# Kernel optimization log

Hardware: AMD Instinct MI355X
Metric: run time of the kernel (lower is better)

## Reference

```python
import jax, jax.numpy as jnp
import numpy as np

LRELU_SLOPE = 0.2  # PyG GATConv default negative_slope
LN_EPS = 1e-5


def _layer_norm(x, g, b):
    mu = x.mean(-1, keepdims=True)
    var = x.var(-1, keepdims=True)
    return (x - mu) / jnp.sqrt(var + LN_EPS) * g + b


def _gat_conv(x, src, dst, W, a_src, a_dst, bias, heads, out_c, concat):
    # PyG GATConv (eval mode, self-loops already appended to src/dst).
    N = x.shape[0]
    h = (x @ W).reshape(N, heads, out_c)            # [N,H,C]
    e_src = (h * a_src).sum(-1)                     # [N,H]
    e_dst = (h * a_dst).sum(-1)                     # [N,H]
    e = jax.nn.leaky_relu(e_src[src] + e_dst[dst], LRELU_SLOPE)  # [E,H]
    # segment softmax over incoming edges of each dst node
    m = jax.ops.segment_max(e, dst, num_segments=N)
    m = jnp.where(jnp.isfinite(m), m, 0.0)
    w = jnp.exp(e - m[dst])
    denom = jax.ops.segment_sum(w, dst, num_segments=N)
    alpha = w / (denom[dst] + 1e-16)                # [E,H]
    out = jax.ops.segment_sum(h[src] * alpha[:, :, None], dst, num_segments=N)  # [N,H,C]
    out = out.reshape(N, heads * out_c) if concat else out.mean(1)
    return out + bias


def setup_inputs() -> dict:
    key = jax.random.key(0)
    ks = jax.random.split(key, 16)
    N, E, F0, Hd, H, G = 50000, 800000, 32, 32, 4, 512
    s = 0.1
    nrm = lambda k, shape: jax.random.normal(k, shape, jnp.float32) * s
    d = {}
    d['x'] = jax.random.normal(ks[0], (N, F0), jnp.float32)
    d['edge_index'] = jax.random.randint(ks[1], (2, E), 0, N)
    d['batch'] = jnp.sort(jax.random.randint(ks[2], (N,), 0, G))
    d['num_graphs'] = G
    # layer 1: F0 -> (Hd, H heads, concat)
    d['W1'] = nrm(ks[3], (F0, H * Hd)); d['as1'] = nrm(ks[4], (H, Hd)); d['ad1'] = nrm(ks[5], (H, Hd))
    d['b1'] = jnp.zeros((H * Hd,)); d['g1'] = jnp.ones((H * Hd,)); d['be1'] = jnp.zeros((H * Hd,))
    # layer 2: H*Hd -> (Hd, H heads, concat)
    d['W2'] = nrm(ks[6], (H * Hd, H * Hd)); d['as2'] = nrm(ks[7], (H, Hd)); d['ad2'] = nrm(ks[8], (H, Hd))
    d['b2'] = jnp.zeros((H * Hd,)); d['g2'] = jnp.ones((H * Hd,)); d['be2'] = jnp.zeros((H * Hd,))
    # layer 3: H*Hd -> (Hd, 1 head, mean)
    d['W3'] = nrm(ks[9], (H * Hd, Hd)); d['as3'] = nrm(ks[10], (1, Hd)); d['ad3'] = nrm(ks[11], (1, Hd))
    d['b3'] = jnp.zeros((Hd,)); d['g3'] = jnp.ones((Hd,)); d['be3'] = jnp.zeros((Hd,))
    # classifier MLP: 2*Hd -> Hd -> Hd//2 -> 1 (torch Linear [out,in])
    d['cW1'] = nrm(ks[12], (Hd, 2 * Hd)); d['cb1'] = jnp.zeros((Hd,))
    d['cW2'] = nrm(ks[13], (Hd // 2, Hd)); d['cb2'] = jnp.zeros((Hd // 2,))
    d['cW3'] = nrm(ks[14], (1, Hd // 2)); d['cb3'] = jnp.zeros((1,))
    return d


def reference(x, edge_index, batch, num_graphs,
              W1, as1, ad1, b1, g1, be1,
              W2, as2, ad2, b2, g2, be2,
              W3, as3, ad3, b3, g3, be3,
              cW1, cb1, cW2, cb2, cW3, cb3):
    N = x.shape[0]
    loop = jnp.arange(N)
    src = jnp.concatenate([edge_index[0], loop])
    dst = jnp.concatenate([edge_index[1], loop])
    h = jax.nn.elu(_layer_norm(_gat_conv(x, src, dst, W1, as1, ad1, b1, 4, 32, True), g1, be1))
    h = jax.nn.elu(_layer_norm(_gat_conv(h, src, dst, W2, as2, ad2, b2, 4, 32, True), g2, be2))
    h = jax.nn.elu(_layer_norm(_gat_conv(h, src, dst, W3, as3, ad3, b3, 1, 32, False), g3, be3))
    cnt = jax.ops.segment_sum(jnp.ones((N,), h.dtype), batch, num_segments=num_graphs)
    x_mean = jax.ops.segment_sum(h, batch, num_segments=num_graphs) / jnp.maximum(cnt, 1.0)[:, None]
    x_max = jax.ops.segment_max(h, batch, num_segments=num_graphs)
    f = jnp.concatenate([x_mean, x_max], axis=1)        # [G, 64]
    f = jax.nn.relu(f @ cW1.T + cb1)
    f = jax.nn.relu(f @ cW2.T + cb2)
    return (f @ cW3.T + cb3).squeeze(-1)                 # [G]
```

## Files before the change

kernel.cpp:

```cpp
#include <hip/hip_runtime.h>
#include <hip/hip_fp16.h>
#include <math.h>

#define CDIV(a, b) (((a) + (b) - 1) / (b))
#define SCAN_BS 1024
#define NBUK 512
#define ATILE 4096

typedef _Float16 f16x8 __attribute__((ext_vector_type(8)));
typedef float f32x4 __attribute__((ext_vector_type(4)));

__device__ __forceinline__ unsigned encf(float v) {
    unsigned u = __float_as_uint(v);
    return (u & 0x80000000u) ? ~u : (u | 0x80000000u);
}
__device__ __forceinline__ float decf(unsigned k) {
    unsigned u = (k & 0x80000000u) ? (k ^ 0x80000000u) : ~k;
    return __uint_as_float(u);
}

__device__ __forceinline__ float lrelu(float v) {
    return v > 0.f ? v : 0.2f * v;
}

__global__ __launch_bounds__(256) void gemm_kernel(
    const float* __restrict__ X, const float* __restrict__ W,
    float* __restrict__ Y, int M, int K, int Nout) {
    int idx = blockIdx.x * blockDim.x + threadIdx.x;
    if (idx >= M * Nout) return;
    int row = idx / Nout;
    int col = idx - row * Nout;
    const float* xr = X + (size_t)row * K;
    const float* wc = W + col;
    float acc = 0.f;
    for (int k = 0; k < K; k += 4) {
        float4 xv = *(const float4*)(xr + k);
        acc += xv.x * wc[(size_t)(k + 0) * Nout];
        acc += xv.y * wc[(size_t)(k + 1) * Nout];
        acc += xv.z * wc[(size_t)(k + 2) * Nout];
        acc += xv.w * wc[(size_t)(k + 3) * Nout];
    }
    Y[idx] = acc;
}

__device__ __forceinline__ void wprep_one(const float* __restrict__ W,
                                          __half* __restrict__ Whf, int K,
                                          int NOUT, int idx) {
    int NK = K / 32;
    int l = idx & 63, f = idx >> 6;
    int ks = f % NK, tt = f / NK;
    int quad = l >> 4, c15 = l & 15;
    _Float16 v[8];
#pragma unroll
    for (int j = 0; j < 8; ++j) {
        int k = ks * 32 + quad * 8 + j;
        int n = tt * 16 + c15;
        v[j] = (_Float16)W[(size_t)k * NOUT + n];
    }
    *(uint4*)(Whf + (size_t)idx * 8) = *(uint4*)v;
}

__device__ __forceinline__ void wprep_one_lds(const float* __restrict__ W,
                                              __half* Whf, int K, int NOUT,
                                              int idx) {
    int NK = K / 32;
    int l = idx & 63, f = idx >> 6;
    int ks = f % NK, tt = f / NK;
    int quad = l >> 4, c15 = l & 15;
    _Float16 v[8];
#pragma unroll
    for (int j = 0; j < 8; ++j) {
        int k = ks * 32 + quad * 8 + j;
        int n = tt * 16 + c15;
        v[j] = (_Float16)W[(size_t)k * NOUT + n];
    }
    *(uint4*)(Whf + (size_t)idx * 8) = *(uint4*)v;
}

__device__ __forceinline__ f16x8 loadA(const float* p) {
    float4 lo = *(const float4*)p;
    float4 hi = *(const float4*)(p + 4);
    f16x8 a;
    a[0] = (_Float16)lo.x; a[1] = (_Float16)lo.y;
    a[2] = (_Float16)lo.z; a[3] = (_Float16)lo.w;
    a[4] = (_Float16)hi.x; a[5] = (_Float16)hi.y;
    a[6] = (_Float16)hi.z; a[7] = (_Float16)hi.w;
    return a;
}
__device__ __forceinline__ f16x8 loadA(const __half* p) {
    return *(const f16x8*)p;
}

template <int K, int NOUT, int HH, typename XT, typename BP>
__device__ __forceinline__ void gemm_attn_body(
    const XT* __restrict__ X, const BP* bp, __half* __restrict__ Y,
    const float* __restrict__ a_src, const float* __restrict__ a_dst,
    float* __restrict__ es, float* __restrict__ ed, int M, int blk) {
    constexpr int NK = K / 32, NT = NOUT / 16;
    static_assert(NT == 2 * HH, "32 channels per head assumed");
    int wave = threadIdx.x >> 6, lane = threadIdx.x & 63;
    int quad = lane >> 4, c15 = lane & 15;
    int row0 = (blk * 4 + wave) * 16;
    if (row0 >= M) return;
    int arow = row0 + c15;
    if (arow >= M) arow = M - 1;
    const XT* xr = X + (size_t)arow * K + quad * 8;
    f32x4 acc[NT];
#pragma unroll
    for (int t = 0; t < NT; ++t) {
        acc[t][0] = 0.f; acc[t][1] = 0.f; acc[t][2] = 0.f; acc[t][3] = 0.f;
    }
#pragma unroll
    for (int ks = 0; ks < NK; ++ks) {
        f16x8 a = loadA(xr + ks * 32);
#pragma unroll
        for (int t = 0; t < NT; ++t) {
            f16x8 b = *(const f16x8*)&bp[((t * NK + ks) * 64 + lane) * 8];
            acc[t] = __builtin_amdgcn_mfma_f32_16x16x32_f16(a, b, acc[t],
                                                            0, 0, 0);
        }
    }
#pragma unroll
    for (int r = 0; r < 4; ++r) {
        int row = row0 + quad * 4 + r;
        if (row < M) {
#pragma unroll
            for (int t = 0; t < NT; ++t)
                Y[(size_t)row * NOUT + t * 16 + c15] = (__half)acc[t][r];
        }
    }
    float asv[NT], adv[NT];
#pragma unroll
    for (int t = 0; t < NT; ++t) {
        asv[t] = a_src[t * 16 + c15];
        adv[t] = a_dst[t * 16 + c15];
    }
#pragma unroll
    for (int h = 0; h < HH; ++h) {
#pragma unroll
        for (int r = 0; r < 4; ++r) {
            float s = acc[2 * h][r] * asv[2 * h] +
                      acc[2 * h + 1][r] * asv[2 * h + 1];
            float dd = acc[2 * h][r] * adv[2 * h] +
                       acc[2 * h + 1][r] * adv[2 * h + 1];
#pragma unroll
            for (int off = 8; off >= 1; off >>= 1) {
                s += __shfl_xor(s, off);
                dd += __shfl_xor(dd, off);
            }
            int row = row0 + quad * 4 + r;
            if (row < M) {
                if (c15 == 0) es[row * HH + h] = s;
                if (c15 == 1) ed[row * HH + h] = dd;
            }
        }
    }
}

__global__ __launch_bounds__(256) void binA1_kernel(
    const int* __restrict__ ei, int E, int* __restrict__ ghist,
    int* __restrict__ pool0, int poolN, const float* __restrict__ W1,
    const float* __restrict__ W2, const float* __restrict__ W3,
    __half* __restrict__ wh2, __half* __restrict__ wh3,
    int* __restrict__ rowptr, int N, int nhist, int nwp,
    const float* __restrict__ x, __half* __restrict__ Qh,
    const float* __restrict__ as1, const float* __restrict__ ad1,
    float* __restrict__ es, float* __restrict__ ed) {
    __shared__ int lh[NBUK];
    __shared__ __half wlds[512 * 8];
    int t = threadIdx.x;
    if (blockIdx.x >= nhist + nwp) {
        for (int i = t; i < 512; i += 256)
            wprep_one_lds(W1, wlds, 32, 128, i);
        __syncthreads();
        gemm_attn_body<32, 128, 4>(x, wlds, Qh, as1, ad1, es, ed, N,
                                   blockIdx.x - nhist - nwp);
        return;
    }
    if (blockIdx.x >= nhist) {
        int idx = (blockIdx.x - nhist) * 256 + t;
        if (idx == 0) rowptr[N] = E + N;
        if (idx < 2048) {
            wprep_one(W2, wh2, 128, 128, idx);
        } else if (idx < 2560) {
            wprep_one(W3, wh3, 128, 32, idx - 2048);
        }
        return;
    }
    int gid = blockIdx.x * 256 + t;
    if (gid < poolN) pool0[gid] = 0;
    for (int i = t; i < NBUK; i += 256) lh[i] = 0;
    __syncthreads();
    int base = blockIdx.x * ATILE;
#pragma unroll 4
    for (int j = 0; j < ATILE / 256; ++j) {
        int idx = base + t + 256 * j;
        if (idx < E) atomicAdd(&lh[ei[E + idx] >> 7], 1);
    }
    __syncthreads();
    int* gh = ghist + (size_t)blockIdx.x * NBUK;
    for (int i = t; i < NBUK; i += 256) gh[i] = lh[i];
}

__global__ __launch_bounds__(64) void binA2a_kernel(
    int* __restrict__ ghist, int* __restrict__ tot, int nblk) {
    int b = blockIdx.x;
    int lane = threadIdx.x;
    int accb = 0;
    for (int chunk = 0; chunk < nblk; chunk += 64) {
        int i = chunk + lane;
        int v = (i < nblk) ? ghist[(size_t)i * NBUK + b] : 0;
        int s = v;
        for (int off = 1; off < 64; off <<= 1) {
            int tv = __shfl_up(s, off);
            if (lane >= off) s += tv;
        }
        if (i < nblk) ghist[(size_t)i * NBUK + b] = s - v + accb;
        accb += __shfl(s, 63);
    }
    if (lane == 0) tot[b] = accb;
}

__device__ __forceinline__ void bucketScan(const int* __restrict__ tot,
                                           int* __restrict__ sc, int t,
                                           int& a0, int& a1, int& excl) {
    a0 = tot[2 * t];
    a1 = tot[2 * t + 1];
    int pair = a0 + a1;
    sc[t] = pair;
    __syncthreads();
#pragma unroll
    for (int off = 1; off < 256; off <<= 1) {
        int v = (t >= off) ? sc[t - off] : 0;
        __syncthreads();
        sc[t] += v;
        __syncthreads();
    }
    excl = sc[t] - pair;
}

__global__ __launch_bounds__(256) void binA3_kernel(
    const int* __restrict__ ei, int E, const int* __restrict__ ghist,
    const int* __restrict__ tot, unsigned* __restrict__ ebuf) {
    __shared__ int lcur[NBUK];
    __shared__ int sc[256];
    int t = threadIdx.x;
    int a0, a1, excl;
    bucketScan(tot, sc, t, a0, a1, excl);
    const int* gh = ghist + (size_t)blockIdx.x * NBUK;
    lcur[2 * t] = gh[2 * t] + excl;
    lcur[2 * t + 1] = gh[2 * t + 1] + excl + a0;
    __syncthreads();
    int base = blockIdx.x * ATILE;
#pragma unroll 4
    for (int j = 0; j < ATILE / 256; ++j) {
        int idx = base + t + 256 * j;
        if (idx < E) {
            int s = ei[idx];
            int d = ei[E + idx];
            int pos = atomicAdd(&lcur[d >> 7], 1);
            ebuf[pos] = ((unsigned)d << 16) | (unsigned)s;
        }
    }
}

__global__ __launch_bounds__(256) void binB_kernel(
    const unsigned* __restrict__ ebuf, const int* __restrict__ tot,
    int* __restrict__ rowptr, int* __restrict__ csrc, int N) {
    __shared__ int cnt_[128];
    __shared__ int pre[128];
    __shared__ int lcur[128];
    __shared__ int sc[256];
    __shared__ int begS;
    int b = blockIdx.x;
    int t = threadIdx.x;
    int n0 = b << 7;
    int totb = tot[b];
    if (t < 128) cnt_[t] = 0;
    int a0, a1, excl;
    bucketScan(tot, sc, t, a0, a1, excl);
    if (t == (b >> 1)) begS = (b & 1) ? (excl + a0) : excl;
    __syncthreads();
    int beg = begS, end = begS + totb;
    for (int i = beg + t; i < end; i += 256)
        atomicAdd(&cnt_[(ebuf[i] >> 16) - n0], 1);
    __syncthreads();
    if (t < 128) pre[t] = (n0 + t < N) ? (cnt_[t] + 1) : 0;
    __syncthreads();
    for (int off = 1; off < 128; off <<= 1) {
        int v = 0;
        if (t < 128 && t >= off) v = pre[t - off];
        __syncthreads();
        if (t < 128) pre[t] += v;
        __syncthreads();
    }
    int cbase = beg + n0;
    if (t < 128 && n0 + t < N) {
        int ex = pre[t] - (cnt_[t] + 1);
        int rp = cbase + ex;
        rowptr[n0 + t] = rp;
        csrc[rp] = n0 + t;
        lcur[t] = rp + 1;
    }
    __syncthreads();
    for (int i = beg + t; i < end; i += 256) {
        unsigned e = ebuf[i];
        int d = (int)(e >> 16) - n0;
        int s = (int)(e & 0xFFFFu);
        int pos = atomicAdd(&lcur[d], 1);
        csrc[pos] = s;
    }
}

__global__ __launch_bounds__(256) void attn_kernel(
    const float* __restrict__ h, const float* __restrict__ a_src,
    const float* __restrict__ a_dst, float* __restrict__ es,
    float* __restrict__ ed, int N, int H, int C) {
    int idx = blockIdx.x * blockDim.x + threadIdx.x;
    if (idx >= N * H) return;
    int n = idx / H;
    int hh = idx - n * H;
    const float* hp = h + (size_t)n * H * C + (size_t)hh * C;
    const float* ap = a_src + hh * C;
    const float* bp = a_dst + hh * C;
    float s = 0.f, d = 0.f;
    for (int c = 0; c < C; c += 4) {
        float4 hv = *(const float4*)(hp + c);
        float4 av = *(const float4*)(ap + c);
        float4 bv = *(const float4*)(bp + c);
        s += hv.x * av.x + hv.y * av.y + hv.z * av.z + hv.w * av.w;
        d += hv.x * bv.x + hv.y * bv.y + hv.z * bv.z + hv.w * bv.w;
    }
    es[idx] = s;
    ed[idx] = d;
}

__global__ __launch_bounds__(256) void deg_kernel(const int* __restrict__ ei,
                                                  int E,
                                                  int* __restrict__ deg) {
    int e = blockIdx.x * blockDim.x + threadIdx.x;
    if (e >= E) return;
    atomicAdd(&deg[ei[E + e]], 1);
}

__global__ __launch_bounds__(SCAN_BS) void scan1_kernel(
    const int* __restrict__ deg, int* __restrict__ rowptr,
    int* __restrict__ bsum, int N) {
    __shared__ int tmp[SCAN_BS];
    int tid = threadIdx.x;
    int gid = blockIdx.x * SCAN_BS + tid;
    int v = (gid < N) ? (deg[gid] + 1) : 0;
    tmp[tid] = v;
    __syncthreads();
    for (int off = 1; off < SCAN_BS; off <<= 1) {
        int t = (tid >= off) ? tmp[tid - off] : 0;
        __syncthreads();
        tmp[tid] += t;
        __syncthreads();
    }
    if (gid < N) rowptr[gid] = tmp[tid] - v;
    if (tid == SCAN_BS - 1) bsum[blockIdx.x] = tmp[tid];
}

__global__ void scan2_kernel(int* __restrict__ bsum, int nb) {
    if (threadIdx.x == 0 && blockIdx.x == 0) {
        int acc = 0;
        for (int i = 0; i < nb; ++i) {
            int t = bsum[i];
            bsum[i] = acc;
            acc += t;
        }
    }
}

__global__ __launch_bounds__(SCAN_BS) void scan3_kernel(
    int* __restrict__ rowptr, int* __restrict__ cursor,
    int* __restrict__ csrc, const int* __restrict__ bsum, int N, int total) {
    int gid = blockIdx.x * SCAN_BS + threadIdx.x;
    if (gid < N) {
        int v = rowptr[gid] + bsum[blockIdx.x];
        rowptr[gid] = v;
        cursor[gid] = v + 1;
        csrc[v] = gid;
    }
    if (gid == 0) rowptr[N] = total;
}

__global__ __launch_bounds__(256) void scatter_kernel(
    const int* __restrict__ ei, int E, int* __restrict__ cursor,
    int* __restrict__ csrc) {
    int e = blockIdx.x * blockDim.x + threadIdx.x;
    if (e >= E) return;
    int s = ei[e];
    int d = ei[E + e];
    int pos = atomicAdd(&cursor[d], 1);
    csrc[pos] = s;
}

template <int NOUT, int HH>
__global__ __launch_bounds__(256) void aggr_gemm_kernel(
    const int* __restrict__ rowptr, const int* __restrict__ csrc,
    const __half* __restrict__ h, const float* __restrict__ es,
    const float* __restrict__ ed, const float* __restrict__ bias,
    const float* __restrict__ gam, const float* __restrict__ bet,
    const __half* __restrict__ Whf, __half* __restrict__ Y,
    const float* __restrict__ a_src, const float* __restrict__ a_dst,
    float* __restrict__ es_o, float* __restrict__ ed_o, int N) {
    constexpr int D = 128, H = 4;
    constexpr int NK = 4, NT = NOUT / 16;
    static_assert(NT == 2 * HH, "32 channels per head assumed");
    __shared__ __half lds[16][136];
    int tid = threadIdx.x;
    int r = tid >> 4;
    int cl = tid & 15;
    int d = blockIdx.x * 16 + r;
    int c = cl * 8;
    if (d < N) {
        int hh = cl >> 2;
        float edv = ed[d * H + hh];
        float acc[8];
#pragma unroll
        for (int i = 0; i < 8; ++i) acc[i] = 0.f;
        float l = 0.f;
        int k = rowptr[d], end = rowptr[d + 1];
        for (; k + 8 <= end; k += 8) {
            int s[8];
#pragma unroll
            for (int j = 0; j < 8; ++j) s[j] = csrc[k + j];
            float e[8];
#pragma unroll
            for (int j = 0; j < 8; ++j) e[j] = es[s[j] * H + hh];
            uint4 u[8];
#pragma unroll
            for (int j = 0; j < 8; ++j)
                u[j] = *(const uint4*)(h + (size_t)s[j] * D + c);
#pragma unroll
            for (int j = 0; j < 8; ++j) {
                float w = __expf(lrelu(e[j] + edv));
                l += w;
                const __half2* hp = (const __half2*)&u[j];
#pragma unroll
                for (int i = 0; i < 4; ++i) {
                    float2 f = __half22float2(hp[i]);
                    acc[2 * i] += w * f.x;
                    acc[2 * i + 1] += w * f.y;
                }
            }
        }
        for (; k + 4 <= end; k += 4) {
            int s[4];
#pragma unroll
            for (int j = 0; j < 4; ++j) s[j] = csrc[k + j];
            float e[4];
#pragma unroll
            for (int j = 0; j < 4; ++j) e[j] = es[s[j] * H + hh];
            uint4 u[4];
#pragma unroll
            for (int j = 0; j < 4; ++j)
                u[j] = *(const uint4*)(h + (size_t)s[j] * D + c);
#pragma unroll
            for (int j = 0; j < 4; ++j) {
                float w = __expf(lrelu(e[j] + edv));
                l += w;
                const __half2* hp = (const __half2*)&u[j];
#pragma unroll
                for (int i = 0; i < 4; ++i) {
                    float2 f = __half22float2(hp[i]);
                    acc[2 * i] += w * f.x;
                    acc[2 * i + 1] += w * f.y;
                }
            }
        }
        for (; k < end; ++k) {
            int s = csrc[k];
            float w = __expf(lrelu(es[s * H + hh] + edv));
            uint4 u = *(const uint4*)(h + (size_t)s * D + c);
            l += w;
            const __half2* hp = (const __half2*)&u;
#pragma unroll
            for (int i = 0; i < 4; ++i) {
                float2 f = __half22float2(hp[i]);
                acc[2 * i] += w * f.x;
                acc[2 * i + 1] += w * f.y;
            }
        }
        float rl = 1.f / (l + 1e-16f);
        float4 b0 = *(const float4*)(bias + c);
        float4 b1 = *(const float4*)(bias + c + 4);
        float v[8];
        v[0] = acc[0] * rl + b0.x; v[1] = acc[1] * rl + b0.y;
        v[2] = acc[2] * rl + b0.z; v[3] = acc[3] * rl + b0.w;
        v[4] = acc[4] * rl + b1.x; v[5] = acc[5] * rl + b1.y;
        v[6] = acc[6] * rl + b1.z; v[7] = acc[7] * rl + b1.w;
        float sm = 0.f, ssum = 0.f;
#pragma unroll
        for (int i = 0; i < 8; ++i) { sm += v[i]; ssum += v[i] * v[i]; }
#pragma unroll
        for (int off = 1; off <= 8; off <<= 1) {
            sm += __shfl_xor(sm, off);
            ssum += __shfl_xor(ssum, off);
        }
        float mean = sm / D;
        float var = ssum / D - mean * mean;
        float rstd = rsqrtf(var + 1e-5f);
        float4 g0 = *(const float4*)(gam + c);
        float4 g1 = *(const float4*)(gam + c + 4);
        float4 t0 = *(const float4*)(bet + c);
        float4 t1 = *(const float4*)(bet + c + 4);
        float gv[8] = {g0.x, g0.y, g0.z, g0.w, g1.x, g1.y, g1.z, g1.w};
        float tv[8] = {t0.x, t0.y, t0.z, t0.w, t1.x, t1.y, t1.z, t1.w};
        __half2 p[4];
#pragma unroll
        for (int i = 0; i < 4; ++i) {
            float o0 = (v[2 * i] - mean) * rstd * gv[2 * i] + tv[2 * i];
            float o1 = (v[2 * i + 1] - mean) * rstd * gv[2 * i + 1] +
                       tv[2 * i + 1];
            o0 = o0 > 0.f ? o0 : expm1f(o0);
            o1 = o1 > 0.f ? o1 : expm1f(o1);
            p[i] = __floats2half2_rn(o0, o1);
        }
        uint4 uo;
        uo.x = *(unsigned*)&p[0];
        uo.y = *(unsigned*)&p[1];
        uo.z = *(unsigned*)&p[2];
        uo.w = *(unsigned*)&p[3];
        *(uint4*)&lds[r][c] = uo;
    } else {
        uint4 z = {0u, 0u, 0u, 0u};
        *(uint4*)&lds[r][c] = z;
    }
    __syncthreads();
    int wave = tid >> 6, lane = tid & 63;
    int quad = lane >> 4, c15 = lane & 15;
    int row0 = blockIdx.x * 16;
    int t0 = (NT == 8) ? 2 * wave : 0;
    bool act = (NT == 8) || (wave == 0);
    if (act) {
        f32x4 a0c, a1c;
        a0c[0] = 0.f; a0c[1] = 0.f; a0c[2] = 0.f; a0c[3] = 0.f;
        a1c = a0c;
#pragma unroll
        for (int ks = 0; ks < NK; ++ks) {
            f16x8 a = *(f16x8*)&lds[c15][quad * 8 + ks * 32];
            f16x8 b0 = *(const f16x8*)(Whf +
                        (size_t)((t0 * NK + ks) * 64 + lane) * 8);
            f16x8 b1 = *(const f16x8*)(Whf +
                        (size_t)(((t0 + 1) * NK + ks) * 64 + lane) * 8);
            a0c = __builtin_amdgcn_mfma_f32_16x16x32_f16(a, b0, a0c, 0, 0, 0);
            a1c = __builtin_amdgcn_mfma_f32_16x16x32_f16(a, b1, a1c, 0, 0, 0);
        }
#pragma unroll
        for (int rr = 0; rr < 4; ++rr) {
            int row = row0 + quad * 4 + rr;
            if (row < N) {
                Y[(size_t)row * NOUT + t0 * 16 + c15] = (__half)a0c[rr];
                Y[(size_t)row * NOUT + (t0 + 1) * 16 + c15] = (__half)a1c[rr];
            }
        }
        int hd = t0 >> 1;
        float as0 = a_src[t0 * 16 + c15], as1 = a_src[(t0 + 1) * 16 + c15];
        float ad0 = a_dst[t0 * 16 + c15], ad1 = a_dst[(t0 + 1) * 16 + c15];
#pragma unroll
        for (int rr = 0; rr < 4; ++rr) {
            float s = a0c[rr] * as0 + a1c[rr] * as1;
            float dd = a0c[rr] * ad0 + a1c[rr] * ad1;
#pragma unroll
            for (int off = 8; off >= 1; off >>= 1) {
                s += __shfl_xor(s, off);
                dd += __shfl_xor(dd, off);
            }
            int row = row0 + quad * 4 + rr;
            if (row < N) {
                if (c15 == 0) es_o[row * HH + hd] = s;
                if (c15 == 1) ed_o[row * HH + hd] = dd;
            }
        }
    }
}

__global__ __launch_bounds__(256) void aggr_ln32_pool_kernel(
    const int* __restrict__ rowptr, const int* __restrict__ csrc,
    const __half* __restrict__ h, const float* __restrict__ es,
    const float* __restrict__ ed, const float* __restrict__ bias,
    const float* __restrict__ gam, const float* __restrict__ bet,
    const int* __restrict__ batch, float* __restrict__ psum,
    unsigned* __restrict__ pmax, float* __restrict__ cnt, int N) {
    constexpr int D = 32;
    __shared__ float lsum[2][32];
    __shared__ unsigned lmax[2][32];
    __shared__ float lcnt[2];
    __shared__ int g0s;
    int tid = threadIdx.x;
    int d = (blockIdx.x * 256 + tid) >> 3;
    int cl = tid & 7;
    int c = cl * 4;
    int dbase = blockIdx.x * 32;
    if (tid < 64) {
        lsum[tid >> 5][tid & 31] = 0.f;
        lmax[tid >> 5][tid & 31] = 0u;
    }
    if (tid < 2) lcnt[tid] = 0.f;
    if (tid == 0) g0s = batch[dbase < N ? dbase : (N - 1)];
    __syncthreads();
    int g0 = g0s;
    if (d < N) {
        float edv = ed[d];
        float acc[4] = {0.f, 0.f, 0.f, 0.f};
        float l = 0.f;
        int k = rowptr[d], end = rowptr[d + 1];
        for (; k + 8 <= end; k += 8) {
            int s[8];
#pragma unroll
            for (int j = 0; j < 8; ++j) s[j] = csrc[k + j];
            float e[8];
#pragma unroll
            for (int j = 0; j < 8; ++j) e[j] = es[s[j]];
            uint2 u[8];
#pragma unroll
            for (int j = 0; j < 8; ++j)
                u[j] = *(const uint2*)(h + (size_t)s[j] * D + c);
#pragma unroll
            for (int j = 0; j < 8; ++j) {
                float w = __expf(lrelu(e[j] + edv));
                l += w;
                float2 f0 = __half22float2(*(__half2*)&u[j].x);
                float2 f1 = __half22float2(*(__half2*)&u[j].y);
                acc[0] += w * f0.x; acc[1] += w * f0.y;
                acc[2] += w * f1.x; acc[3] += w * f1.y;
            }
        }
        for (; k + 4 <= end; k += 4) {
            int s[4];
#pragma unroll
            for (int j = 0; j < 4; ++j) s[j] = csrc[k + j];
            float e[4];
#pragma unroll
            for (int j = 0; j < 4; ++j) e[j] = es[s[j]];
            uint2 u[4];
#pragma unroll
            for (int j = 0; j < 4; ++j)
                u[j] = *(const uint2*)(h + (size_t)s[j] * D + c);
#pragma unroll
            for (int j = 0; j < 4; ++j) {
                float w = __expf(lrelu(e[j] + edv));
                l += w;
                float2 f0 = __half22float2(*(__half2*)&u[j].x);
                float2 f1 = __half22float2(*(__half2*)&u[j].y);
                acc[0] += w * f0.x; acc[1] += w * f0.y;
                acc[2] += w * f1.x; acc[3] += w * f1.y;
            }
        }
        for (; k < end; ++k) {
            int s = csrc[k];
            float w = __expf(lrelu(es[s] + edv));
            uint2 u = *(const uint2*)(h + (size_t)s * D + c);
            l += w;
            float2 f0 = __half22float2(*(__half2*)&u.x);
            float2 f1 = __half22float2(*(__half2*)&u.y);
            acc[0] += w * f0.x; acc[1] += w * f0.y;
            acc[2] += w * f1.x; acc[3] += w * f1.y;
        }
        float rl = 1.f / (l + 1e-16f);
        float4 b4 = *(const float4*)(bias + c);
        float v0 = acc[0] * rl + b4.x;
        float v1 = acc[1] * rl + b4.y;
        float v2 = acc[2] * rl + b4.z;
        float v3 = acc[3] * rl + b4.w;
        float sm = v0 + v1 + v2 + v3;
        float ssum = v0 * v0 + v1 * v1 + v2 * v2 + v3 * v3;
#pragma unroll
        for (int off = 1; off <= 4; off <<= 1) {
            sm += __shfl_xor(sm, off);
            ssum += __shfl_xor(ssum, off);
        }
        float mean = sm / D;
        float var = ssum / D - mean * mean;
        float rstd = rsqrtf(var + 1e-5f);
        float4 g4 = *(const float4*)(gam + c);
        float4 t4 = *(const float4*)(bet + c);
        float o0 = (v0 - mean) * rstd * g4.x + t4.x;
        float o1 = (v1 - mean) * rstd * g4.y + t4.y;
        float o2 = (v2 - mean) * rstd * g4.z + t4.z;
        float o3 = (v3 - mean) * rstd * g4.w + t4.w;
        o0 = o0 > 0.f ? o0 : expm1f(o0);
        o1 = o1 > 0.f ? o1 : expm1f(o1);
        o2 = o2 > 0.f ? o2 : expm1f(o2);
        o3 = o3 > 0.f ? o3 : expm1f(o3);
        int g = batch[d];
        int goff = g - g0;
        if (goff >= 0 && goff < 2) {
            atomicAdd(&lsum[goff][c + 0], o0);
            atomicAdd(&lsum[goff][c + 1], o1);
            atomicAdd(&lsum[goff][c + 2], o2);
            atomicAdd(&lsum[goff][c + 3], o3);
            atomicMax(&lmax[goff][c + 0], encf(o0));
            atomicMax(&lmax[goff][c + 1], encf(o1));
            atomicMax(&lmax[goff][c + 2], encf(o2));
            atomicMax(&lmax[goff][c + 3], encf(o3));
            if (cl == 0) atomicAdd(&lcnt[goff], 1.0f);
        } else {
            atomicAdd(&psum[g * D + c + 0], o0);
            atomicAdd(&psum[g * D + c + 1], o1);
            atomicAdd(&psum[g * D + c + 2], o2);
            atomicAdd(&psum[g * D + c + 3], o3);
            atomicMax(&pmax[g * D + c + 0], encf(o0));
            atomicMax(&pmax[g * D + c + 1], encf(o1));
            atomicMax(&pmax[g * D + c + 2], encf(o2));
            atomicMax(&pmax[g * D + c + 3], encf(o3));
            if (cl == 0) atomicAdd(&cnt[g], 1.0f);
        }
    }
    __syncthreads();
    if (tid < 64) {
        int go = tid >> 5, cc = tid & 31;
        unsigned m = lmax[go][cc];
        if (m != 0u) {
            int gg = g0 + go;
            atomicAdd(&psum[gg * D + cc], lsum[go][cc]);
            atomicMax(&pmax[gg * D + cc], m);
            if (cc == 0) atomicAdd(&cnt[gg], lcnt[go]);
        }
    }
}

__global__ __launch_bounds__(256) void aggr_csr_kernel(
    const int* __restrict__ rowptr, const int* __restrict__ csrc,
    const float* __restrict__ h, const float* __restrict__ es,
    const float* __restrict__ ed, float* __restrict__ outp, int N, int H,
    int C) {
    int D = H * C;
    int wave = (blockIdx.x * blockDim.x + threadIdx.x) >> 6;
    int lane = threadIdx.x & 63;
    if (wave >= N) return;
    int d = wave;
    int c0 = lane, c1 = lane + 64;
    bool a0 = c0 < D, a1 = c1 < D;
    int h0 = a0 ? c0 / C : 0;
    int h1 = a1 ? c1 / C : 0;
    float edv0 = a0 ? ed[d * H + h0] : 0.f;
    float edv1 = a1 ? ed[d * H + h1] : 0.f;
    float m0 = -INFINITY, m1 = -INFINITY;
    float l0 = 0.f, l1 = 0.f, acc0 = 0.f, acc1 = 0.f;
    int beg = rowptr[d], end = rowptr[d + 1];
    for (int k = beg; k < end; ++k) {
        int s = csrc[k];
        const float* hp = h + (size_t)s * D;
        if (a0) {
            float v = lrelu(es[s * H + h0] + edv0);
            float nm = fmaxf(m0, v);
            float sc = __expf(m0 - nm);
            float w = __expf(v - nm);
            l0 = l0 * sc + w;
            acc0 = acc0 * sc + w * hp[c0];
            m0 = nm;
        }
        if (a1) {
            float v = lrelu(es[s * H + h1] + edv1);
            float nm = fmaxf(m1, v);
            float sc = __expf(m1 - nm);
            float w = __expf(v - nm);
            l1 = l1 * sc + w;
            acc1 = acc1 * sc + w * hp[c1];
            m1 = nm;
        }
    }
    if (a0) outp[(size_t)d * D + c0] = acc0 / (l0 + 1e-16f);
    if (a1) outp[(size_t)d * D + c1] = acc1 / (l1 + 1e-16f);
}

__global__ __launch_bounds__(64) void ln_elu_kernel(
    const float* __restrict__ in, const float* __restrict__ bias,
    const float* __restrict__ gam, const float* __restrict__ bet,
    float* __restrict__ outp, int D) {
    int n = blockIdx.x;
    int lane = threadIdx.x;
    int c0 = lane, c1 = lane + 64;
    bool a0 = c0 < D, a1 = c1 < D;
    float v0 = 0.f, v1 = 0.f;
    if (a0) v0 = in[(size_t)n * D + c0] + bias[c0];
    if (a1) v1 = in[(size_t)n * D + c1] + bias[c1];
    float s = v0 + v1;
    float ss = v0 * v0 + v1 * v1;
    for (int off = 32; off; off >>= 1) {
        s += __shfl_xor(s, off);
        ss += __shfl_xor(ss, off);
    }
    float mean = s / D;
    float var = ss / D - mean * mean;
    float rstd = rsqrtf(var + 1e-5f);
    if (a0) {
        float o = (v0 - mean) * rstd * gam[c0] + bet[c0];
        outp[(size_t)n * D + c0] = o > 0.f ? o : expm1f(o);
    }
    if (a1) {
        float o = (v1 - mean) * rstd * gam[c1] + bet[c1];
        outp[(size_t)n * D + c1] = o > 0.f ? o : expm1f(o);
    }
}

__global__ __launch_bounds__(256) void pool_kernel(
    const float* __restrict__ h, const int* __restrict__ batch, int N, int C,
    float* __restrict__ psum, unsigned* __restrict__ pmax,
    float* __restrict__ cnt) {
    int idx = blockIdx.x * blockDim.x + threadIdx.x;
    if (idx >= N * C) return;
    int n = idx / C;
    int c = idx - n * C;
    int g = batch[n];
    float v = h[(size_t)n * C + c];
    atomicAdd(&psum[g * C + c], v);
    atomicMax(&pmax[g * C + c], encf(v));
    if (c == 0) atomicAdd(&cnt[g], 1.0f);
}

__global__ __launch_bounds__(64) void mlp_kernel(
    const float* __restrict__ psum, const unsigned* __restrict__ pmax,
    const float* __restrict__ cnt, const float* __restrict__ cW1,
    const float* __restrict__ cb1, const float* __restrict__ cW2,
    const float* __restrict__ cb2, const float* __restrict__ cW3,
    const float* __restrict__ cb3, float* __restrict__ outp, int C) {
    __shared__ float f[64];
    __shared__ float t1[32];
    __shared__ float t2[16];
    int g = blockIdx.x;
    int t = threadIdx.x;
    float c = fmaxf(cnt[g], 1.0f);
    if (t < C) {
        f[t] = psum[g * C + t] / c;
    } else if (t < 2 * C) {
        unsigned k = pmax[g * C + (t - C)];
        f[t] = (k == 0u) ? -INFINITY : decf(k);
    }
    __syncthreads();
    if (t < 32) {
        float a = cb1[t];
        for (int i = 0; i < 64; ++i) a += f[i] * cW1[t * 64 + i];
        t1[t] = fmaxf(a, 0.f);
    }
    __syncthreads();
    if (t < 16) {
        float a = cb2[t];
        for (int i = 0; i < 32; ++i) a += t1[i] * cW2[t * 32 + i];
        t2[t] = fmaxf(a, 0.f);
    }
    __syncthreads();
    if (t == 0) {
        float a = cb3[0];
        for (int i = 0; i < 16; ++i) a += t2[i] * cW3[i];
        outp[g] = a;
    }
}

extern "C" void kernel_launch(void* const* d_in, const int* in_sizes, int n_in,
                              void* d_out, int out_size, void* d_ws,
                              size_t ws_size, hipStream_t stream) {
    const float* x = (const float*)d_in[0];
    const int* ei = (const int*)d_in[1];
    const int* batch = (const int*)d_in[2];
    const float* W1 = (const float*)d_in[4];
    const float* as1 = (const float*)d_in[5];
    const float* ad1 = (const float*)d_in[6];
    const float* b1 = (const float*)d_in[7];
    const float* g1 = (const float*)d_in[8];
    const float* be1 = (const float*)d_in[9];
    const float* W2 = (const float*)d_in[10];
    const float* as2 = (const float*)d_in[11];
    const float* ad2 = (const float*)d_in[12];
    const float* b2 = (const float*)d_in[13];
    const float* g2 = (const float*)d_in[14];
    const float* be2 = (const float*)d_in[15];
    const float* W3 = (const float*)d_in[16];
    const float* as3 = (const float*)d_in[17];
    const float* ad3 = (const float*)d_in[18];
    const float* b3 = (const float*)d_in[19];
    const float* g3 = (const float*)d_in[20];
    const float* be3 = (const float*)d_in[21];
    const float* cW1 = (const float*)d_in[22];
    const float* cb1 = (const float*)d_in[23];
    const float* cW2 = (const float*)d_in[24];
    const float* cb2 = (const float*)d_in[25];
    const float* cW3 = (const float*)d_in[26];
    const float* cb3 = (const float*)d_in[27];

    const int N = in_sizes[2];
    const int E = in_sizes[1] / 2;
    const int F0 = in_sizes[0] / N;
    const int Hd = in_sizes[19];
    const int H = in_sizes[5] / Hd;
    const int D = H * Hd;
    const int H3 = in_sizes[17] / Hd;
    const int G = out_size;
    const int EN = E + N;
    const bool shapes_ok = (F0 == 32 && Hd == 32 && H == 4 && D == 128 &&
                            H3 == 1 && N <= 65536);

    char* w = (char*)d_ws;
    size_t off = 0;
    auto carve = [&](size_t bytes) -> void* {
        void* p = w + off;
        off = (off + bytes + 255) & ~(size_t)255;
        return p;
    };
    float* Q = (float*)carve((size_t)N * D * 4);
    __half* Qh = (__half*)Q;
    float* R = (float*)carve((size_t)N * D * 4);
    float* P = (float*)carve((size_t)N * D * 4);
    __half* Ph = (__half*)P;
    float* es1 = (float*)carve((size_t)N * H * 4);
    float* ed1 = (float*)carve((size_t)N * H * 4);
    float* es2 = (float*)carve((size_t)N * H * 4);
    float* ed2 = (float*)carve((size_t)N * H * 4);
    int* rowptr = (int*)carve((size_t)(N + 1) * 4);
    int* cursor = (int*)carve((size_t)N * 4);
    int* csrc = (int*)carve((size_t)EN * 4);
    int* bsum = (int*)carve((size_t)CDIV(N, SCAN_BS) * 4);
    const int nblkA = CDIV(E, ATILE);
    int* ghist = (int*)carve((size_t)nblkA * NBUK * 4);
    int* tot = (int*)carve((size_t)NBUK * 4);
    unsigned* ebuf = (unsigned*)carve((size_t)E * 4);
    __half* wh2 = (__half*)carve((size_t)8 * 4 * 64 * 8 * 2);
    __half* wh3 = (__half*)carve((size_t)2 * 4 * 64 * 8 * 2);
    float* psum = (float*)carve((size_t)G * Hd * 4);
    unsigned* pmax = (unsigned*)carve((size_t)G * Hd * 4);
    float* cnt = (float*)carve((size_t)G * 4);
    (void)ws_size;
    (void)n_in;

    const int BLK = 256;
    const int nb = CDIV(N, SCAN_BS);
    const int poolInts = G * Hd * 2 + G;

    if (shapes_ok) {
        const int nwp = 10;
        const int ngemm1 = CDIV(N, 64);
        binA1_kernel<<<nblkA + nwp + ngemm1, 256, 0, stream>>>(
            ei, E, ghist, (int*)psum, poolInts, W1, W2, W3, wh2, wh3,
            rowptr, N, nblkA, nwp, x, Qh, as1, ad1, es1, ed1);
        binA2a_kernel<<<NBUK, 64, 0, stream>>>(ghist, tot, nblkA);
        binA3_kernel<<<nblkA, 256, 0, stream>>>(ei, E, ghist, tot, ebuf);
        binB_kernel<<<CDIV(N, 128), 256, 0, stream>>>(ebuf, tot, rowptr,
                                                      csrc, N);
        aggr_gemm_kernel<128, 4><<<CDIV(N, 16), 256, 0, stream>>>(
            rowptr, csrc, Qh, es1, ed1, b1, g1, be1, wh2, Ph, as2, ad2,
            es2, ed2, N);
        aggr_gemm_kernel<32, 1><<<CDIV(N, 16), 256, 0, stream>>>(
            rowptr, csrc, Ph, es2, ed2, b2, g2, be2, wh3, Qh, as3, ad3,
            es1, ed1, N);
        aggr_ln32_pool_kernel<<<CDIV(N, 32), 256, 0, stream>>>(
            rowptr, csrc, Qh, es1, ed1, b3, g3, be3, batch, psum, pmax,
            cnt, N);
    } else {
        float* es = es1;
        float* ed = ed1;
        hipMemsetAsync(psum, 0, (size_t)G * Hd * 4, stream);
        hipMemsetAsync(pmax, 0, (size_t)G * Hd * 4, stream);
        hipMemsetAsync(cnt, 0, (size_t)G * 4, stream);
        hipMemsetAsync(cursor, 0, (size_t)N * 4, stream);
        deg_kernel<<<CDIV(E, BLK), BLK, 0, stream>>>(ei, E, cursor);
        scan1_kernel<<<nb, SCAN_BS, 0, stream>>>(cursor, rowptr, bsum, N);
        scan2_kernel<<<1, 64, 0, stream>>>(bsum, nb);
        scan3_kernel<<<nb, SCAN_BS, 0, stream>>>(rowptr, cursor, csrc, bsum, N, EN);
        scatter_kernel<<<CDIV(E, BLK), BLK, 0, stream>>>(ei, E, cursor, csrc);
        gemm_kernel<<<CDIV(N * D, BLK), BLK, 0, stream>>>(x, W1, Q, N, F0, D);
        attn_kernel<<<CDIV(N * H, BLK), BLK, 0, stream>>>(Q, as1, ad1, es, ed, N, H, Hd);
        aggr_csr_kernel<<<CDIV(N, 4), BLK, 0, stream>>>(rowptr, csrc, Q, es, ed, R, N, H, Hd);
        ln_elu_kernel<<<N, 64, 0, stream>>>(R, b1, g1, be1, P, D);
        gemm_kernel<<<CDIV(N * D, BLK), BLK, 0, stream>>>(P, W2, Q, N, D, D);
        attn_kernel<<<CDIV(N * H, BLK), BLK, 0, stream>>>(Q, as2, ad2, es, ed, N, H, Hd);
        aggr_csr_kernel<<<CDIV(N, 4), BLK, 0, stream>>>(rowptr, csrc, Q, es, ed, R, N, H, Hd);
        ln_elu_kernel<<<N, 64, 0, stream>>>(R, b2, g2, be2, P, D);
        gemm_kernel<<<CDIV(N * Hd, BLK), BLK, 0, stream>>>(P, W3, Q, N, D, Hd);
        attn_kernel<<<CDIV(N * H3, BLK), BLK, 0, stream>>>(Q, as3, ad3, es, ed, N, H3, Hd);
        aggr_csr_kernel<<<CDIV(N, 4), BLK, 0, stream>>>(rowptr, csrc, Q, es, ed, R, N, H3, Hd);
        ln_elu_kernel<<<N, 64, 0, stream>>>(R, b3, g3, be3, P, Hd);
        pool_kernel<<<CDIV(N * Hd, BLK), BLK, 0, stream>>>(P, batch, N, Hd, psum, pmax, cnt);
    }

    mlp_kernel<<<G, 64, 0, stream>>>(psum, pmax, cnt, cW1, cb1, cW2, cb2, cW3,
                                     cb3, (float*)d_out, Hd);
}
```

Baseline: 264.0 us.

## Balance edge aggregation within block via shared work queue of 8-edge chunks

```diff
diff --git a/kernel.cpp b/kernel.cpp
--- a/kernel.cpp
+++ b/kernel.cpp
@@ -409,89 +409,97 @@
     constexpr int D = 128, H = 4;
     constexpr int NK = 4, NT = NOUT / 16;
     static_assert(NT == 2 * HH, "32 channels per head assumed");
-    __shared__ __half lds[16][136];
+    __shared__ float accS[16][132];
+    __shared__ float lsumS[16][4];
+    __shared__ __half ldsA[16][136];
+    __shared__ int begS[16], endS[16], chunkBase[17];
+    __shared__ int qctr;
     int tid = threadIdx.x;
     int r = tid >> 4;
     int cl = tid & 15;
-    int d = blockIdx.x * 16 + r;
     int c = cl * 8;
-    if (d < N) {
-        int hh = cl >> 2;
-        float edv = ed[d * H + hh];
-        float acc[8];
-#pragma unroll
-        for (int i = 0; i < 8; ++i) acc[i] = 0.f;
-        float l = 0.f;
-        int k = rowptr[d], end = rowptr[d + 1];
-        for (; k + 8 <= end; k += 8) {
-            int s[8];
-#pragma unroll
-            for (int j = 0; j < 8; ++j) s[j] = csrc[k + j];
-            float e[8];
-#pragma unroll
-            for (int j = 0; j < 8; ++j) e[j] = es[s[j] * H + hh];
-            uint4 u[8];
-#pragma unroll
-            for (int j = 0; j < 8; ++j)
-                u[j] = *(const uint4*)(h + (size_t)s[j] * D + c);
-#pragma unroll
-            for (int j = 0; j < 8; ++j) {
-                float w = __expf(lrelu(e[j] + edv));
-                l += w;
-                const __half2* hp = (const __half2*)&u[j];
-#pragma unroll
-                for (int i = 0; i < 4; ++i) {
-                    float2 f = __half22float2(hp[i]);
-                    acc[2 * i] += w * f.x;
-                    acc[2 * i + 1] += w * f.y;
-                }
-            }
-        }
-        for (; k + 4 <= end; k += 4) {
-            int s[4];
-#pragma unroll
-            for (int j = 0; j < 4; ++j) s[j] = csrc[k + j];
-            float e[4];
-#pragma unroll
-            for (int j = 0; j < 4; ++j) e[j] = es[s[j] * H + hh];
-            uint4 u[4];
-#pragma unroll
-            for (int j = 0; j < 4; ++j)
-                u[j] = *(const uint4*)(h + (size_t)s[j] * D + c);
-#pragma unroll
-            for (int j = 0; j < 4; ++j) {
-                float w = __expf(lrelu(e[j] + edv));
-                l += w;
-                const __half2* hp = (const __half2*)&u[j];
-#pragma unroll
-                for (int i = 0; i < 4; ++i) {
-                    float2 f = __half22float2(hp[i]);
-                    acc[2 * i] += w * f.x;
-                    acc[2 * i + 1] += w * f.y;
-                }
-            }
-        }
-        for (; k < end; ++k) {
-            int s = csrc[k];
-            float w = __expf(lrelu(es[s * H + hh] + edv));
-            uint4 u = *(const uint4*)(h + (size_t)s * D + c);
-            l += w;
-            const __half2* hp = (const __half2*)&u;
+    int hh = cl >> 2;
+    int d0 = blockIdx.x * 16;
+    for (int i = tid; i < 16 * 132; i += 256) ((float*)accS)[i] = 0.f;
+    if (tid < 64) lsumS[tid >> 2][tid & 3] = 0.f;
+    if (tid < 16) {
+        int dd = d0 + tid;
+        begS[tid] = (dd < N) ? rowptr[dd] : 0;
+        endS[tid] = (dd < N) ? rowptr[dd + 1] : 0;
+    }
+    if (tid == 0) qctr = 0;
+    __syncthreads();
+    if (tid == 0) {
+        int a = 0;
+        for (int i = 0; i < 16; ++i) {
+            chunkBase[i] = a;
+            a += (endS[i] - begS[i] + 7) >> 3;
+        }
+        chunkBase[16] = a;
+    }
+    __syncthreads();
+    int T = chunkBase[16];
+    int gleader = (tid & 63) & ~15;
+    while (true) {
+        int ci = 0;
+        if (cl == 0) ci = atomicAdd(&qctr, 1);
+        ci = __shfl(ci, gleader);
+        if (ci >= T) break;
+        int ld = 0;
+        while (chunkBase[ld + 1] <= ci) ++ld;
+        int dd = d0 + ld;
+        float edv = ed[dd * H + hh];
+        int kb = begS[ld] + ((ci - chunkBase[ld]) << 3);
+        int ke = endS[ld];
+        int s[8];
+#pragma unroll
+        for (int j = 0; j < 8; ++j) {
+            int kk = kb + j;
+            s[j] = csrc[kk < ke ? kk : kb];
+        }
+        float e[8];
+#pragma unroll
+        for (int j = 0; j < 8; ++j) e[j] = es[s[j] * H + hh];
+        uint4 u[8];
+#pragma unroll
+        for (int j = 0; j < 8; ++j)
+            u[j] = *(const uint4*)(h + (size_t)s[j] * D + c);
+        float a[8];
+#pragma unroll
+        for (int i = 0; i < 8; ++i) a[i] = 0.f;
+        float lp = 0.f;
+#pragma unroll
+        for (int j = 0; j < 8; ++j) {
+            float w = (kb + j < ke) ? __expf(lrelu(e[j] + edv)) : 0.f;
+            lp += w;
+            const __half2* hp = (const __half2*)&u[j];
 #pragma unroll
             for (int i = 0; i < 4; ++i) {
                 float2 f = __half22float2(hp[i]);
-                acc[2 * i] += w * f.x;
-                acc[2 * i + 1] += w * f.y;
+                a[2 * i] += w * f.x;
+                a[2 * i + 1] += w * f.y;
             }
         }
+#pragma unroll
+        for (int i = 0; i < 8; ++i) atomicAdd(&accS[ld][c + i], a[i]);
+        if ((cl & 3) == 0) atomicAdd(&lsumS[ld][hh], lp);
+    }
+    __syncthreads();
+    int d = d0 + r;
+    if (d < N) {
+        float l = lsumS[r][hh];
         float rl = 1.f / (l + 1e-16f);
         float4 b0 = *(const float4*)(bias + c);
         float4 b1 = *(const float4*)(bias + c + 4);
         float v[8];
-        v[0] = acc[0] * rl + b0.x; v[1] = acc[1] * rl + b0.y;
-        v[2] = acc[2] * rl + b0.z; v[3] = acc[3] * rl + b0.w;
-        v[4] = acc[4] * rl + b1.x; v[5] = acc[5] * rl + b1.y;
-        v[6] = acc[6] * rl + b1.z; v[7] = acc[7] * rl + b1.w;
+        v[0] = accS[r][c + 0] * rl + b0.x;
+        v[1] = accS[r][c + 1] * rl + b0.y;
+        v[2] = accS[r][c + 2] * rl + b0.z;
+        v[3] = accS[r][c + 3] * rl + b0.w;
+        v[4] = accS[r][c + 4] * rl + b1.x;
+        v[5] = accS[r][c + 5] * rl + b1.y;
+        v[6] = accS[r][c + 6] * rl + b1.z;
+        v[7] = accS[r][c + 7] * rl + b1.w;
         float sm = 0.f, ssum = 0.f;
 #pragma unroll
         for (int i = 0; i < 8; ++i) { sm += v[i]; ssum += v[i] * v[i]; }
@@ -524,10 +532,10 @@
         uo.y = *(unsigned*)&p[1];
         uo.z = *(unsigned*)&p[2];
         uo.w = *(unsigned*)&p[3];
-        *(uint4*)&lds[r][c] = uo;
+        *(uint4*)&ldsA[r][c] = uo;
     } else {
         uint4 z = {0u, 0u, 0u, 0u};
-        *(uint4*)&lds[r][c] = z;
+        *(uint4*)&ldsA[r][c] = z;
     }
     __syncthreads();
     int wave = tid >> 6, lane = tid & 63;
@@ -541,7 +549,7 @@
         a1c = a0c;
 #pragma unroll
         for (int ks = 0; ks < NK; ++ks) {
-            f16x8 a = *(f16x8*)&lds[c15][quad * 8 + ks * 32];
+            f16x8 a = *(f16x8*)&ldsA[c15][quad * 8 + ks * 32];
             f16x8 b0 = *(const f16x8*)(Whf +
                         (size_t)((t0 * NK + ks) * 64 + lane) * 8);
             f16x8 b1 = *(const f16x8*)(Whf +
```

New measurement: 397.2 us. 50.4% more time.
